# Performance work log

Measured on AMD Instinct MI355X. Metric: run time of the kernel, lower is better.

## Reference

```python
import jax, jax.numpy as jnp
import numpy as np
import math

C = 64
SCALE = 1.0 / math.sqrt(C * 9)  # BaseConv2d: 1/sqrt(in_channel*k^2), k=3


def _conv(x, w, b=None, pad=0):
    out = jax.lax.conv_general_dilated(
        x, w, window_strides=(1, 1), padding=[(pad, pad), (pad, pad)],
        dimension_numbers=("NCHW", "OIHW", "NCHW"))
    return out if b is None else out + b[None, :, None, None]


def _mod_conv(x, w, b, cond, pad):
    # cond: [B,1,C,1,1]. Original builds per-sample weights W*scale*cond and runs a
    # groups=B conv. Since cond scales the INPUT-channel axis and is spatially
    # constant, conv(x, W*diag(cond_b)) == conv(x*cond_b, W): identical math.
    return _conv(x * cond[:, 0], w * SCALE, b, pad)


def _resblock(x, w2, b2, cond2):
    # w2: [2,C,C,3,3], b2: [2,C], cond2: [2,B,1,C,1,1]
    r = jax.nn.relu(_mod_conv(x, w2[0], b2[0], cond2[0], 1))
    r = _mod_conv(r, w2[1], b2[1], cond2[1], 1)
    return r + x


def _mfe(x, w1, b1, w3, b3, w5, b5, cw1, cw2, fw, fb):
    lrelu = lambda z: jax.nn.leaky_relu(z, 0.01)
    x1 = _conv(lrelu(_conv(x, w1[0], b1[0], 0)), w1[1], b1[1], 0)
    x3 = _conv(lrelu(_conv(x, w3[0], b3[0], 1)), w3[1], b3[1], 1)
    x5 = _conv(lrelu(_conv(x, w5[0], b5[0], 2)), w5[1], b5[1], 2)
    # ChannelAttention: shared SE MLP (1x1 convs, no bias) on max- and avg-pooled stats
    se = lambda z: jnp.einsum("oi,bihw->bohw", cw2, jax.nn.relu(jnp.einsum("oi,bihw->bohw", cw1, z)))
    mx = jnp.max(x, axis=(2, 3), keepdims=True)
    av = jnp.mean(x, axis=(2, 3), keepdims=True)
    xll = jax.nn.sigmoid(se(mx) + se(av))  # [B,C,1,1]
    # FC1 = Linear(1,1) -> Linear(1,1) on the trailing size-1 dim; C1==C2==C3 (same module)
    Cg = fw[1] * (fw[0] * xll + fb[0]) + fb[1]
    return Cg * (x1 + x3 + x5)


def _pms(x, cf1, cf2, map_, res_w, res_b, mw1, mb1, mw3, mb3, mw5, mb5, caw1, caw2, fcw, fcb):
    conds = [cf1[i] for i in range(5)] + [cf2[i] for i in range(4)]
    mfe_after = {1: 0, 3: 1, 5: 2, 7: 3, 8: 4}
    o = x
    for i in range(9):
        o = _resblock(o, res_w[i], res_b[i], conds[i])
        if i in mfe_after:
            j = mfe_after[i]
            o = _mfe(o, mw1[j], mb1[j], mw3[j], mb3[j], mw5[j], mb5[j],
                     caw1[j], caw2[j], fcw[j], fcb[j])
    return o * map_ + x


def setup_inputs() -> dict:
    key = jax.random.key(0)
    ks = jax.random.split(key, 16)
    B, H, W = 4, 128, 128
    d = {}
    d["x"] = jax.random.normal(ks[0], (B, C, H, W), jnp.float32)
    # modulation scales ~1 (EqualLinear bias_init=1)
    d["condition_feature1"] = jax.random.uniform(ks[1], (5, 2, B, 1, C, 1, 1), jnp.float32, 0.5, 1.5)
    d["condition_feature2"] = jax.random.uniform(ks[2], (4, 2, B, 1, C, 1, 1), jnp.float32, 0.5, 1.5)
    d["map"] = jax.random.uniform(ks[3], (B, 1, H, W), jnp.float32)
    d["res_w"] = jax.random.normal(ks[4], (9, 2, C, C, 3, 3), jnp.float32)  # BaseConv2d stores raw randn weight
    d["res_b"] = jax.random.normal(ks[5], (9, 2, C), jnp.float32) * 0.01
    d["mw1"] = jax.random.normal(ks[6], (5, 2, C, C, 1, 1), jnp.float32) * (0.1 * math.sqrt(2.0 / C))
    d["mb1"] = jnp.zeros((5, 2, C), jnp.float32)
    d["mw3"] = jax.random.normal(ks[7], (5, 2, C, C, 3, 3), jnp.float32) * (0.1 * math.sqrt(2.0 / (C * 9)))
    d["mb3"] = jnp.zeros((5, 2, C), jnp.float32)
    d["mw5"] = jax.random.normal(ks[8], (5, 2, C, C, 5, 5), jnp.float32) * (0.1 * math.sqrt(2.0 / (C * 25)))
    d["mb5"] = jnp.zeros((5, 2, C), jnp.float32)
    d["caw1"] = jax.random.normal(ks[9], (5, C // 16, C), jnp.float32) * math.sqrt(2.0 / C)
    d["caw2"] = jax.random.normal(ks[10], (5, C, C // 16), jnp.float32) * math.sqrt(2.0 / (C // 16))
    d["fcw"] = jax.random.normal(ks[11], (5, 2), jnp.float32)
    d["fcb"] = jax.random.normal(ks[12], (5, 2), jnp.float32) * 0.1
    return d


def reference(x, condition_feature1, condition_feature2, map, res_w, res_b,
              mw1, mb1, mw3, mb3, mw5, mb5, caw1, caw2, fcw, fcb):
    return _pms(x, condition_feature1, condition_feature2, map, res_w, res_b,
                mw1, mb1, mw3, mb3, mw5, mb5, caw1, caw2, fcw, fcb)
```

## Files before the change

kernel.cpp:

```cpp
#include <hip/hip_runtime.h>
#include <math.h>

constexpr int B = 4, C = 64, H = 128, W = 128;
constexpr int HW = H * W;
constexpr size_t TOT   = (size_t)B * C * HW;
constexpr float SCALE  = 1.0f / 24.0f;

typedef _Float16 half8 __attribute__((ext_vector_type(8)));
typedef _Float16 half4v __attribute__((ext_vector_type(4)));
typedef float floatx4 __attribute__((ext_vector_type(4)));

constexpr size_t A_RES = 0;
constexpr size_t A_M1  = 2654208;
constexpr size_t A_M3  = 2695168;
constexpr size_t A_M5  = 3063808;
constexpr size_t A_TOT = 4087808;

__global__ __launch_bounds__(256) void wt_kernel(
    const float* __restrict__ rw, const float* __restrict__ mw1,
    const float* __restrict__ mw3, const float* __restrict__ mw5,
    const float* __restrict__ cf1, const float* __restrict__ cf2,
    _Float16* __restrict__ wt)
{
    size_t e = (size_t)blockIdx.x * 256 + threadIdx.x;
    const float* src; int K; float scale; int l;
    if (e < A_M1) {
        int cb = (int)(e / 36864); l = (int)(e - (size_t)cb * 36864);
        int conv = cb >> 2, b = cb & 3;
        src = rw + (size_t)conv * 36864; K = 3;
        int icw = l & 7, l15 = (l >> 3) & 15, q = (l >> 7) & 3;
        int mt = (l >> 9) & 3, h = (l >> 11) & 1, kk = l >> 12;
        int oc = mt * 16 + l15, ic = h * 32 + q * 8 + icw;
        int kh = kk / 3, kw = kk - kh * 3;
        float cond = (conv < 10) ? cf1[(size_t)(conv * 4 + b) * 64 + ic]
                                 : cf2[(size_t)((conv - 10) * 4 + b) * 64 + ic];
        wt[e] = (_Float16)(src[((oc * C + ic) * 3 + kh) * 3 + kw] * SCALE * cond);
        return;
    } else if (e < A_M3) {
        int e2 = (int)(e - A_M1); int conv = e2 / 4096; l = e2 - conv * 4096;
        src = mw1 + (size_t)conv * 4096; K = 1; scale = 1.f;
    } else if (e < A_M5) {
        int e2 = (int)(e - A_M3); int conv = e2 / 36864; l = e2 - conv * 36864;
        src = mw3 + (size_t)conv * 36864; K = 3; scale = 1.f;
    } else {
        int e2 = (int)(e - A_M5); int conv = e2 / 102400; l = e2 - conv * 102400;
        src = mw5 + (size_t)conv * 102400; K = 5; scale = 1.f;
    }
    int j   = l & 7;
    int l15 = (l >> 3) & 15;
    int q   = (l >> 7) & 3;
    int mt  = (l >> 9) & 3;
    int h   = (l >> 11) & 1;
    int kk  = l >> 12;
    int oc = mt * 16 + l15, ic = h * 32 + q * 8 + j;
    int kh = kk / K, kw = kk - kh * K;
    wt[e] = (_Float16)(src[((oc * C + ic) * K + kh) * K + kw] * scale);
}

__global__ __launch_bounds__(256) void xcvt_kernel(
    const float* __restrict__ x, _Float16* __restrict__ xh)
{
    __shared__ _Float16 s[64 * 72];
    const int b = blockIdx.y;
    const size_t p0 = (size_t)blockIdx.x * 64;
    const int t = threadIdx.x, px = t & 63, cg0 = t >> 6;
#pragma unroll
    for (int k = 0; k < 16; ++k) {
        int c = cg0 * 16 + k;
        s[px * 72 + c] = (_Float16)x[((size_t)(b * 64 + c)) * HW + p0 + px];
    }
    __syncthreads();
#pragma unroll
    for (int k = 0; k < 2; ++k) {
        int idx = k * 256 + t;
        int pxw = idx >> 3, o8 = idx & 7;
        uint4 v = *(const uint4*)&s[pxw * 72 + o8 * 8];
        *(uint4*)&xh[((size_t)b * HW + p0 + pxw) * 64 + o8 * 8] = v;
    }
}

__global__ __launch_bounds__(256) void init_kernel(unsigned* __restrict__ st)
{
    int i = blockIdx.x * 256 + threadIdx.x;
    if (i < 5 * 512) st[i] = 0u;
}

__device__ __forceinline__ unsigned fenc(float f) {
    unsigned b = __float_as_uint(f);
    return (b & 0x80000000u) ? ~b : (b | 0x80000000u);
}
__device__ __forceinline__ float fdec(unsigned u) {
    unsigned b = (u & 0x80000000u) ? (u & 0x7fffffffu) : ~u;
    return __uint_as_float(b);
}

__device__ __forceinline__ void loadAo(const _Float16* __restrict__ base,
                                       int og, int q, int l15, uint4* dst)
{
    const uint4* p = (const uint4*)base;
#pragma unroll
    for (int h = 0; h < 2; ++h)
#pragma unroll
        for (int m = 0; m < 2; ++m)
            dst[h * 2 + m] = p[(h * 4 + og * 2 + m) * 64 + q * 16 + l15];
}

template <int IWs, int NPXP>
__device__ __forceinline__ void mstep_og(const unsigned int* __restrict__ s_b,
    const uint4* a, floatx4 (&acc)[2][4], int ph, int l15, int q,
    int kh, int kw, int off)
{
#pragma unroll
    for (int h = 0; h < 2; ++h) {
        half8 af0 = __builtin_bit_cast(half8, a[h * 2 + 0]);
        half8 af1 = __builtin_bit_cast(half8, a[h * 2 + 1]);
#pragma unroll
        for (int ng = 0; ng < 4; ++ng) {
            int row = 4 * ph + ng + kh + off;
            int px = row * IWs + l15 + kw + off;
            half8 bf = __builtin_bit_cast(half8, ((const uint4*)s_b)[(h * 4 + q) * NPXP + px]);
            acc[0][ng] = __builtin_amdgcn_mfma_f32_16x16x32_f16(af0, bf, acc[0][ng], 0, 0, 0);
            acc[1][ng] = __builtin_amdgcn_mfma_f32_16x16x32_f16(af1, bf, acc[1][ng], 0, 0, 0);
        }
    }
}

template <bool STATS>
__global__ __launch_bounds__(512, 1) void fres_kernel(
    const _Float16* __restrict__ in, const _Float16* __restrict__ w0a,
    const _Float16* __restrict__ w1a,
    const float* __restrict__ bias0, const float* __restrict__ bias1,
    unsigned* __restrict__ umax, float* __restrict__ fsum,
    _Float16* __restrict__ out)
{
    constexpr int NIN = 401;
    constexpr int RNP = 329;
    __shared__ __align__(16) unsigned s_in[NIN * 32];
    __shared__ __align__(16) unsigned s_r[RNP * 32];
    __shared__ float s_stat[2][8][64];

    const int tid = threadIdx.x;
    const int bx = blockIdx.x, b = blockIdx.y;
    const int y0 = (bx >> 3) * 16, x0 = (bx & 7) * 16;
    const _Float16* w0 = w0a + (size_t)b * 36864;
    const _Float16* w1 = w1a + (size_t)b * 36864;
    const int lane = tid & 63, wv = tid >> 6;
    const int pg = wv & 3, og = wv >> 2;
    const int l15 = lane & 15, q = lane >> 4;

    uint4 a0[4], a1[4];
    loadAo(w0, og, q, l15, a0);

    for (int idx = tid; idx < 400 * 8; idx += 512) {
        int px = idx >> 3, o8 = idx & 7;
        int r = px / 20, cix = px - r * 20;
        int gy = y0 + r - 2, gx = x0 + cix - 2;
        uint4 v = {0u, 0u, 0u, 0u};
        if (gy >= 0 && gy < H && gx >= 0 && gx < W)
            v = *(const uint4*)&in[((size_t)b * HW + (size_t)gy * W + gx) * 64 + o8 * 8];
        ((uint4*)s_in)[o8 * NIN + px] = v;
    }
    __syncthreads();

    int spb[6], pval[6];
#pragma unroll
    for (int t = 0; t < 6; ++t) {
        int p = (pg * 6 + t) * 16 + l15;
        pval[t] = p;
        int pc = p < 324 ? p : 0;
        int jr = pc / 18, jc = pc - jr * 18;
        spb[t] = jr * 20 + jc;
    }

    floatx4 acc1[2][6] = {};
#pragma unroll
    for (int g = 0; g < 9; ++g) {
        uint4* cur = (g & 1) ? a1 : a0;
        uint4* nxt = (g & 1) ? a0 : a1;
        const _Float16* np = (g < 8) ? w0 + (size_t)(g + 1) * 4096 : w1;
        loadAo(np, og, q, l15, nxt);
        __builtin_amdgcn_sched_barrier(0);
        const int kh = g / 3, kw = g - kh * 3;
#pragma unroll
        for (int h = 0; h < 2; ++h) {
            half8 af0 = __builtin_bit_cast(half8, cur[h * 2 + 0]);
            half8 af1 = __builtin_bit_cast(half8, cur[h * 2 + 1]);
#pragma unroll
            for (int t = 0; t < 6; ++t) {
                half8 bf = __builtin_bit_cast(half8,
                    ((const uint4*)s_in)[(h * 4 + q) * NIN + spb[t] + kh * 20 + kw]);
                acc1[0][t] = __builtin_amdgcn_mfma_f32_16x16x32_f16(af0, bf, acc1[0][t], 0, 0, 0);
                acc1[1][t] = __builtin_amdgcn_mfma_f32_16x16x32_f16(af1, bf, acc1[1][t], 0, 0, 0);
            }
        }
    }

#pragma unroll
    for (int t = 0; t < 6; ++t) {
        int p = pval[t];
        if (p < 324) {
            int jr = p / 18, jc = p - jr * 18;
            bool valid = (unsigned)(y0 + jr - 1) < (unsigned)H &&
                         (unsigned)(x0 + jc - 1) < (unsigned)W;
#pragma unroll
            for (int m = 0; m < 2; ++m) {
                int oc0 = og * 32 + m * 16 + q * 4;
                float4 bv = *(const float4*)(bias0 + oc0);
                float v0 = 0.f, v1 = 0.f, v2 = 0.f, v3 = 0.f;
                if (valid) {
                    v0 = fmaxf(acc1[m][t][0] + bv.x, 0.f);
                    v1 = fmaxf(acc1[m][t][1] + bv.y, 0.f);
                    v2 = fmaxf(acc1[m][t][2] + bv.z, 0.f);
                    v3 = fmaxf(acc1[m][t][3] + bv.w, 0.f);
                }
                half4v hv = { (_Float16)v0, (_Float16)v1, (_Float16)v2, (_Float16)v3 };
                int o8r = og * 4 + m * 2 + (q >> 1);
                ((uint2*)s_r)[(o8r * RNP + p) * 2 + (q & 1)] = __builtin_bit_cast(uint2, hv);
            }
        }
    }
    __syncthreads();

    floatx4 acc2[2][4] = {};
#pragma unroll
    for (int g = 0; g < 9; ++g) {
        uint4* cur = (g & 1) ? a0 : a1;
        uint4* nxt = (g & 1) ? a1 : a0;
        if (g < 8) {
            loadAo(w1 + (size_t)(g + 1) * 4096, og, q, l15, nxt);
            __builtin_amdgcn_sched_barrier(0);
        }
        const int kh = g / 3, kw = g - kh * 3;
#pragma unroll
        for (int h = 0; h < 2; ++h) {
            half8 af0 = __builtin_bit_cast(half8, cur[h * 2 + 0]);
            half8 af1 = __builtin_bit_cast(half8, cur[h * 2 + 1]);
#pragma unroll
            for (int ng = 0; ng < 4; ++ng) {
                int sp = (pg * 4 + ng + kh) * 18 + l15 + kw;
                half8 bf = __builtin_bit_cast(half8, ((const uint4*)s_r)[(h * 4 + q) * RNP + sp]);
                acc2[0][ng] = __builtin_amdgcn_mfma_f32_16x16x32_f16(af0, bf, acc2[0][ng], 0, 0, 0);
                acc2[1][ng] = __builtin_amdgcn_mfma_f32_16x16x32_f16(af1, bf, acc2[1][ng], 0, 0, 0);
            }
        }
    }

    float lmax[2][4], lsum[2][4];
    if (STATS) {
#pragma unroll
        for (int m = 0; m < 2; ++m)
#pragma unroll
            for (int r = 0; r < 4; ++r) { lmax[m][r] = -INFINITY; lsum[m][r] = 0.f; }
    }
#pragma unroll
    for (int m = 0; m < 2; ++m) {
        const int oc0 = og * 32 + m * 16 + q * 4;
        const float4 bv = *(const float4*)(bias1 + oc0);
        const int o8r = og * 4 + m * 2 + (q >> 1);
#pragma unroll
        for (int ng = 0; ng < 4; ++ng) {
            const int row = pg * 4 + ng;
            const int spres = (row + 2) * 20 + l15 + 2;
            uint2 ru = ((const uint2*)s_in)[(o8r * NIN + spres) * 2 + (q & 1)];
            half4v rv = __builtin_bit_cast(half4v, ru);
            float v[4];
            v[0] = acc2[m][ng][0] + bv.x + (float)rv[0];
            v[1] = acc2[m][ng][1] + bv.y + (float)rv[1];
            v[2] = acc2[m][ng][2] + bv.z + (float)rv[2];
            v[3] = acc2[m][ng][3] + bv.w + (float)rv[3];
            const size_t off = ((size_t)b * HW + (size_t)(y0 + row) * W + x0 + l15) * 64 + oc0;
            half4v hv = { (_Float16)v[0], (_Float16)v[1], (_Float16)v[2], (_Float16)v[3] };
            *(half4v*)&out[off] = hv;
            if (STATS) {
#pragma unroll
                for (int r = 0; r < 4; ++r) {
                    lmax[m][r] = fmaxf(lmax[m][r], v[r]);
                    lsum[m][r] += v[r];
                }
            }
        }
    }
    if (STATS) {
#pragma unroll
        for (int msk = 1; msk < 16; msk <<= 1) {
#pragma unroll
            for (int m = 0; m < 2; ++m)
#pragma unroll
                for (int r = 0; r < 4; ++r) {
                    lmax[m][r] = fmaxf(lmax[m][r], __shfl_xor(lmax[m][r], msk));
                    lsum[m][r] += __shfl_xor(lsum[m][r], msk);
                }
        }
        if (l15 == 0) {
#pragma unroll
            for (int m = 0; m < 2; ++m)
#pragma unroll
                for (int r = 0; r < 4; ++r) {
                    int oc = og * 32 + m * 16 + q * 4 + r;
                    s_stat[0][wv][oc] = lmax[m][r];
                    s_stat[1][wv][oc] = lsum[m][r];
                }
        }
        __syncthreads();
        if (tid < 64) {
            int oc = tid;
            int w0i = (oc < 32) ? 0 : 4;
            float mv = s_stat[0][w0i][oc], sv = s_stat[1][w0i][oc];
#pragma unroll
            for (int k = 1; k < 4; ++k) {
                mv = fmaxf(mv, s_stat[0][w0i + k][oc]);
                sv += s_stat[1][w0i + k][oc];
            }
            atomicMax(&umax[b * 64 + oc], fenc(mv));
            atomicAdd(&fsum[b * 64 + oc], sv);
        }
    }
}

__global__ __launch_bounds__(256, 2) void mfe1_kernel(
    const _Float16* __restrict__ in,
    const _Float16* __restrict__ w5, const _Float16* __restrict__ w3,
    const _Float16* __restrict__ w1,
    const float* __restrict__ b5, const float* __restrict__ b3,
    const float* __restrict__ b1,
    _Float16* __restrict__ t5, _Float16* __restrict__ t3, _Float16* __restrict__ t1)
{
    constexpr int IWs = 20, NPX = 240, NPXP = 241;
    __shared__ __align__(16) unsigned int s_b[NPXP * 32];

    const int tid = threadIdx.x;
    const int bx = blockIdx.x, b = blockIdx.y;
    const int y0 = (bx >> 3) * 8, x0 = (bx & 7) * 16;
    const int lane = tid & 63, wv = tid >> 6;
    const int ph = wv & 1, og = wv >> 1;
    const int l15 = lane & 15, q = lane >> 4;

    uint4 a0[4], a1[4];
    loadAo(w5, og, q, l15, a0);

    for (int idx = tid; idx < NPX * 8; idx += 256) {
        int px = idx >> 3, o8 = idx & 7;
        int r = px / IWs, cix = px - r * IWs;
        int gy = y0 + r - 2, gx = x0 + cix - 2;
        uint4 v = {0u, 0u, 0u, 0u};
        if (gy >= 0 && gy < H && gx >= 0 && gx < W)
            v = *(const uint4*)&in[((size_t)b * HW + (size_t)gy * W + gx) * 64 + o8 * 8];
        ((uint4*)s_b)[o8 * NPXP + px] = v;
    }
    __syncthreads();

    floatx4 acc[2][4] = {};
    const floatx4 z4 = {0.f, 0.f, 0.f, 0.f};

    auto epi = [&](const float* bias, _Float16* outp, bool reset) {
#pragma unroll
        for (int m = 0; m < 2; ++m) {
            const int oc0 = og * 32 + m * 16 + q * 4;
            const float4 bv = *(const float4*)(bias + oc0);
#pragma unroll
            for (int ng = 0; ng < 4; ++ng) {
                const int y = y0 + 4 * ph + ng, x = x0 + l15;
                const size_t off = ((size_t)b * HW + (size_t)y * W + x) * 64 + oc0;
                float v[4] = { acc[m][ng][0] + bv.x, acc[m][ng][1] + bv.y,
                               acc[m][ng][2] + bv.z, acc[m][ng][3] + bv.w };
#pragma unroll
                for (int r = 0; r < 4; ++r) v[r] = v[r] > 0.f ? v[r] : 0.01f * v[r];
                half4v hv = { (_Float16)v[0], (_Float16)v[1], (_Float16)v[2], (_Float16)v[3] };
                *(half4v*)&outp[off] = hv;
                if (reset) acc[m][ng] = z4;
            }
        }
    };

#pragma unroll
    for (int g = 0; g < 25; ++g) {
        uint4* cur = (g & 1) ? a1 : a0;
        uint4* nxt = (g & 1) ? a0 : a1;
        const _Float16* np = (g + 1 < 25) ? w5 + (size_t)(g + 1) * 4096 : w3;
        loadAo(np, og, q, l15, nxt);
        __builtin_amdgcn_sched_barrier(0);
        mstep_og<IWs, NPXP>(s_b, cur, acc, ph, l15, q, g / 5, g % 5, 0);
    }
    epi(b5, t5, true);
#pragma unroll
    for (int g = 0; g < 9; ++g) {
        uint4* cur = (g & 1) ? a0 : a1;
        uint4* nxt = (g & 1) ? a1 : a0;
        const _Float16* np = (g + 1 < 9) ? w3 + (size_t)(g + 1) * 4096 : w1;
        loadAo(np, og, q, l15, nxt);
        __builtin_amdgcn_sched_barrier(0);
        mstep_og<IWs, NPXP>(s_b, cur, acc, ph, l15, q, g / 3, g % 3, 1);
    }
    epi(b3, t3, true);
    mstep_og<IWs, NPXP>(s_b, a0, acc, ph, l15, q, 0, 0, 2);
    epi(b1, t1, false);
}

__global__ __launch_bounds__(256, 2) void mfe2_kernel(
    const _Float16* __restrict__ t5in, const _Float16* __restrict__ t3in,
    const _Float16* __restrict__ t1in,
    const _Float16* __restrict__ w5, const _Float16* __restrict__ w3,
    const _Float16* __restrict__ w1,
    const float* __restrict__ b5, const float* __restrict__ b3,
    const float* __restrict__ b1,
    const unsigned* __restrict__ umax, const float* __restrict__ fsum,
    const float* __restrict__ caw1, const float* __restrict__ caw2,
    const float* __restrict__ fcwj, const float* __restrict__ fcbj,
    _Float16* __restrict__ o)
{
    constexpr int IWs = 20, NPX = 240, NPXP = 241;
    __shared__ __align__(16) unsigned int s_b[NPXP * 32];
    __shared__ float s_hid[8];

    const int tid = threadIdx.x;
    const int bx = blockIdx.x, b = blockIdx.y;
    const int y0 = (bx >> 3) * 8, x0 = (bx & 7) * 16;
    const int lane = tid & 63, wv = tid >> 6;
    const int ph = wv & 1, og = wv >> 1;
    const int l15 = lane & 15, q = lane >> 4;

    auto stageB = [&](const _Float16* __restrict__ src) {
        for (int idx = tid; idx < NPX * 8; idx += 256) {
            int px = idx >> 3, o8 = idx & 7;
            int r = px / IWs, cix = px - r * IWs;
            int gy = y0 + r - 2, gx = x0 + cix - 2;
            uint4 v = {0u, 0u, 0u, 0u};
            if (gy >= 0 && gy < H && gx >= 0 && gx < W)
                v = *(const uint4*)&src[((size_t)b * HW + (size_t)gy * W + gx) * 64 + o8 * 8];
            ((uint4*)s_b)[o8 * NPXP + px] = v;
        }
    };

    uint4 a0[4], a1[4];
    loadAo(w5, og, q, l15, a0);

    stageB(t5in);
    if (tid < 8) {
        int which = tid >> 2, hh = tid & 3;
        float s = 0.f;
        for (int i = 0; i < 64; ++i) {
            float val = which ? (fsum[b * 64 + i] * (1.f / HW)) : fdec(umax[b * 64 + i]);
            s += caw1[hh * 64 + i] * val;
        }
        s_hid[tid] = fmaxf(s, 0.f);
    }
    __syncthreads();

    floatx4 acc[2][4] = {};

#pragma unroll
    for (int g = 0; g < 25; ++g) {
        uint4* cur = (g & 1) ? a1 : a0;
        uint4* nxt = (g & 1) ? a0 : a1;
        const _Float16* np = (g + 1 < 25) ? w5 + (size_t)(g + 1) * 4096 : w3;
        loadAo(np, og, q, l15, nxt);
        __builtin_amdgcn_sched_barrier(0);
        mstep_og<IWs, NPXP>(s_b, cur, acc, ph, l15, q, g / 5, g % 5, 0);
    }
    __syncthreads();
    stageB(t3in);
    __syncthreads();
#pragma unroll
    for (int g = 0; g < 9; ++g) {
        uint4* cur = (g & 1) ? a0 : a1;
        uint4* nxt = (g & 1) ? a1 : a0;
        const _Float16* np = (g + 1 < 9) ? w3 + (size_t)(g + 1) * 4096 : w1;
        loadAo(np, og, q, l15, nxt);
        __builtin_amdgcn_sched_barrier(0);
        mstep_og<IWs, NPXP>(s_b, cur, acc, ph, l15, q, g / 3, g % 3, 1);
    }
    __syncthreads();
    stageB(t1in);
    __syncthreads();
    mstep_og<IWs, NPXP>(s_b, a0, acc, ph, l15, q, 0, 0, 2);

    float hs[4];
#pragma unroll
    for (int hh = 0; hh < 4; ++hh) hs[hh] = s_hid[hh] + s_hid[4 + hh];
    const float fw0 = fcwj[0], fw1 = fcwj[1], fb0 = fcbj[0], fb1 = fcbj[1];
#pragma unroll
    for (int m = 0; m < 2; ++m) {
        const int oc0 = og * 32 + m * 16 + q * 4;
        const float4 bv5 = *(const float4*)(b5 + oc0);
        const float4 bv3 = *(const float4*)(b3 + oc0);
        const float4 bv1 = *(const float4*)(b1 + oc0);
        float bs[4] = { bv5.x + bv3.x + bv1.x, bv5.y + bv3.y + bv1.y,
                        bv5.z + bv3.z + bv1.z, bv5.w + bv3.w + bv1.w };
        float cg[4];
#pragma unroll
        for (int r = 0; r < 4; ++r) {
            const float4 w2 = *(const float4*)(caw2 + (oc0 + r) * 4);
            float s = w2.x * hs[0] + w2.y * hs[1] + w2.z * hs[2] + w2.w * hs[3];
            float xll = 1.f / (1.f + expf(-s));
            cg[r] = fw1 * (fw0 * xll + fb0) + fb1;
        }
#pragma unroll
        for (int ng = 0; ng < 4; ++ng) {
            const int y = y0 + 4 * ph + ng, x = x0 + l15;
            const size_t off = ((size_t)b * HW + (size_t)y * W + x) * 64 + oc0;
            float v[4];
#pragma unroll
            for (int r = 0; r < 4; ++r) v[r] = (acc[m][ng][r] + bs[r]) * cg[r];
            half4v hv = { (_Float16)v[0], (_Float16)v[1], (_Float16)v[2], (_Float16)v[3] };
            *(half4v*)&o[off] = hv;
        }
    }
}

__global__ __launch_bounds__(256) void final_kernel(
    const _Float16* __restrict__ o, const float* __restrict__ mapp,
    const float* __restrict__ x, float* __restrict__ out)
{
    __shared__ _Float16 s[64 * 72];
    const int b = blockIdx.y;
    const size_t p0 = (size_t)blockIdx.x * 64;
    const int t = threadIdx.x;
#pragma unroll
    for (int k = 0; k < 2; ++k) {
        int idx = k * 256 + t;
        int pxw = idx >> 3, o8 = idx & 7;
        uint4 v = *(const uint4*)&o[((size_t)b * HW + p0 + pxw) * 64 + o8 * 8];
        *(uint4*)&s[pxw * 72 + o8 * 8] = v;
    }
    __syncthreads();
    const int px = t & 63, cg0 = t >> 6;
    const float mv = mapp[(size_t)b * HW + p0 + px];
#pragma unroll
    for (int k = 0; k < 16; ++k) {
        int c = cg0 * 16 + k;
        size_t off = ((size_t)(b * 64 + c)) * HW + p0 + px;
        out[off] = (float)s[px * 72 + c] * mv + x[off];
    }
}

extern "C" void kernel_launch(void* const* d_in, const int* in_sizes, int n_in,
                              void* d_out, int out_size, void* d_ws, size_t ws_size,
                              hipStream_t stream)
{
    const float* x    = (const float*)d_in[0];
    const float* cf1  = (const float*)d_in[1];
    const float* cf2  = (const float*)d_in[2];
    const float* mapp = (const float*)d_in[3];
    const float* rw   = (const float*)d_in[4];
    const float* rb   = (const float*)d_in[5];
    const float* mw1  = (const float*)d_in[6];
    const float* mb1  = (const float*)d_in[7];
    const float* mw3  = (const float*)d_in[8];
    const float* mb3  = (const float*)d_in[9];
    const float* mw5  = (const float*)d_in[10];
    const float* mb5  = (const float*)d_in[11];
    const float* caw1 = (const float*)d_in[12];
    const float* caw2 = (const float*)d_in[13];
    const float* fcw  = (const float*)d_in[14];
    const float* fcb  = (const float*)d_in[15];
    float* out = (float*)d_out;

    _Float16* wta = (_Float16*)d_ws;
    _Float16* hb  = wta + A_TOT;
    _Float16* xh  = hb;
    _Float16* bA  = hb + TOT;
    _Float16* bB  = hb + 2 * TOT;
    _Float16* t5  = hb + 3 * TOT;
    _Float16* t3  = hb + 4 * TOT;
    unsigned* stat = (unsigned*)(hb + 5 * TOT);

    wt_kernel<<<dim3((unsigned)(A_TOT / 256)), 256, 0, stream>>>(rw, mw1, mw3, mw5, cf1, cf2, wta);
    init_kernel<<<dim3(10), 256, 0, stream>>>(stat);
    xcvt_kernel<<<dim3(256, B), 256, 0, stream>>>(x, xh);

    const dim3 fgrid(64, B);
    const dim3 mgrid(128, B);

    const _Float16* cur = xh;
    int mfe_j = 0;
    for (int i = 0; i < 9; ++i) {
        _Float16* nxt = (i & 1) ? bB : bA;
        bool isMfe = (i == 1 || i == 3 || i == 5 || i == 7 || i == 8);
        const _Float16* w0a = wta + A_RES + (size_t)(i * 2 + 0) * 4 * 36864;
        const _Float16* w1a = wta + A_RES + (size_t)(i * 2 + 1) * 4 * 36864;
        unsigned* um = stat + (size_t)mfe_j * 512;
        float* fs = (float*)(stat + (size_t)mfe_j * 512 + 256);
        if (isMfe)
            fres_kernel<true><<<fgrid, 512, 0, stream>>>(
                cur, w0a, w1a, rb + (i * 2 + 0) * C, rb + (i * 2 + 1) * C, um, fs, nxt);
        else
            fres_kernel<false><<<fgrid, 512, 0, stream>>>(
                cur, w0a, w1a, rb + (i * 2 + 0) * C, rb + (i * 2 + 1) * C, nullptr, nullptr, nxt);
        cur = nxt;

        if (isMfe) {
            int j = mfe_j++;
            mfe1_kernel<<<mgrid, 256, 0, stream>>>(
                cur,
                wta + A_M5 + (size_t)(j * 2 + 0) * 102400,
                wta + A_M3 + (size_t)(j * 2 + 0) * 36864,
                wta + A_M1 + (size_t)(j * 2 + 0) * 4096,
                mb5 + (j * 2 + 0) * C, mb3 + (j * 2 + 0) * C, mb1 + (j * 2 + 0) * C,
                t5, t3, xh);
            mfe2_kernel<<<mgrid, 256, 0, stream>>>(
                t5, t3, xh,
                wta + A_M5 + (size_t)(j * 2 + 1) * 102400,
                wta + A_M3 + (size_t)(j * 2 + 1) * 36864,
                wta + A_M1 + (size_t)(j * 2 + 1) * 4096,
                mb5 + (j * 2 + 1) * C, mb3 + (j * 2 + 1) * C, mb1 + (j * 2 + 1) * C,
                um, fs, caw1 + j * 4 * C, caw2 + j * C * 4,
                fcw + j * 2, fcb + j * 2, (_Float16*)cur);
        }
    }
    final_kernel<<<dim3(256, B), 256, 0, stream>>>(cur, mapp, x, out);
}
```

Baseline: 521.2 us.

## Deepen weight prefetch to three buffers and double-buffer LDS B-fragment reads

```diff
diff --git a/kernel.cpp b/kernel.cpp
--- a/kernel.cpp
+++ b/kernel.cpp
@@ -106,9 +106,21 @@
 }
 
 template <int IWs, int NPXP>
-__device__ __forceinline__ void mstep_og(const unsigned int* __restrict__ s_b,
-    const uint4* a, floatx4 (&acc)[2][4], int ph, int l15, int q,
-    int kh, int kw, int off)
+__device__ __forceinline__ void readB8(const unsigned* __restrict__ s_b,
+    int ph, int l15, int q, int kh, int kw, int off, uint4* bf)
+{
+#pragma unroll
+    for (int h = 0; h < 2; ++h)
+#pragma unroll
+        for (int ng = 0; ng < 4; ++ng) {
+            int row = 4 * ph + ng + kh + off;
+            int px = row * IWs + l15 + kw + off;
+            bf[h * 4 + ng] = ((const uint4*)s_b)[(h * 4 + q) * NPXP + px];
+        }
+}
+
+__device__ __forceinline__ void domfma_og(const uint4* a, const uint4* bf,
+                                          floatx4 (&acc)[2][4])
 {
 #pragma unroll
     for (int h = 0; h < 2; ++h) {
@@ -116,13 +128,18 @@
         half8 af1 = __builtin_bit_cast(half8, a[h * 2 + 1]);
 #pragma unroll
         for (int ng = 0; ng < 4; ++ng) {
-            int row = 4 * ph + ng + kh + off;
-            int px = row * IWs + l15 + kw + off;
-            half8 bf = __builtin_bit_cast(half8, ((const uint4*)s_b)[(h * 4 + q) * NPXP + px]);
-            acc[0][ng] = __builtin_amdgcn_mfma_f32_16x16x32_f16(af0, bf, acc[0][ng], 0, 0, 0);
-            acc[1][ng] = __builtin_amdgcn_mfma_f32_16x16x32_f16(af1, bf, acc[1][ng], 0, 0, 0);
-        }
-    }
+            half8 b = __builtin_bit_cast(half8, bf[h * 4 + ng]);
+            acc[0][ng] = __builtin_amdgcn_mfma_f32_16x16x32_f16(af0, b, acc[0][ng], 0, 0, 0);
+            acc[1][ng] = __builtin_amdgcn_mfma_f32_16x16x32_f16(af1, b, acc[1][ng], 0, 0, 0);
+        }
+    }
+}
+
+__device__ __forceinline__ void mfeParams(int g, int& kh, int& kw, int& off)
+{
+    if (g < 25)      { kh = g / 5; kw = g % 5; off = 0; }
+    else if (g < 34) { int ls = g - 25; kh = ls / 3; kw = ls % 3; off = 1; }
+    else             { kh = 0; kw = 0; off = 2; }
 }
 
 template <bool STATS>
@@ -148,8 +165,13 @@
     const int pg = wv & 3, og = wv >> 2;
     const int l15 = lane & 15, q = lane >> 4;
 
-    uint4 a0[4], a1[4];
-    loadAo(w0, og, q, l15, a0);
+    auto aPtrF = [&](int g) -> const _Float16* {
+        return (g < 9) ? w0 + (size_t)g * 4096 : w1 + (size_t)(g - 9) * 4096;
+    };
+
+    uint4 A[3][4];
+    loadAo(aPtrF(0), og, q, l15, A[0]);
+    loadAo(aPtrF(1), og, q, l15, A[1]);
 
     for (int idx = tid; idx < 400 * 8; idx += 512) {
         int px = idx >> 3, o8 = idx & 7;
@@ -175,11 +197,9 @@
     floatx4 acc1[2][6] = {};
 #pragma unroll
     for (int g = 0; g < 9; ++g) {
-        uint4* cur = (g & 1) ? a1 : a0;
-        uint4* nxt = (g & 1) ? a0 : a1;
-        const _Float16* np = (g < 8) ? w0 + (size_t)(g + 1) * 4096 : w1;
-        loadAo(np, og, q, l15, nxt);
+        loadAo(aPtrF(g + 2), og, q, l15, A[(g + 2) % 3]);
         __builtin_amdgcn_sched_barrier(0);
+        const uint4* cur = A[g % 3];
         const int kh = g / 3, kw = g - kh * 3;
 #pragma unroll
         for (int h = 0; h < 2; ++h) {
@@ -221,28 +241,28 @@
     }
     __syncthreads();
 
-    floatx4 acc2[2][4] = {};
-#pragma unroll
-    for (int g = 0; g < 9; ++g) {
-        uint4* cur = (g & 1) ? a0 : a1;
-        uint4* nxt = (g & 1) ? a1 : a0;
-        if (g < 8) {
-            loadAo(w1 + (size_t)(g + 1) * 4096, og, q, l15, nxt);
-            __builtin_amdgcn_sched_barrier(0);
-        }
-        const int kh = g / 3, kw = g - kh * 3;
-#pragma unroll
-        for (int h = 0; h < 2; ++h) {
-            half8 af0 = __builtin_bit_cast(half8, cur[h * 2 + 0]);
-            half8 af1 = __builtin_bit_cast(half8, cur[h * 2 + 1]);
+    auto readB2 = [&](int kh, int kw, uint4* bf) {
+#pragma unroll
+        for (int h = 0; h < 2; ++h)
 #pragma unroll
             for (int ng = 0; ng < 4; ++ng) {
                 int sp = (pg * 4 + ng + kh) * 18 + l15 + kw;
-                half8 bf = __builtin_bit_cast(half8, ((const uint4*)s_r)[(h * 4 + q) * RNP + sp]);
-                acc2[0][ng] = __builtin_amdgcn_mfma_f32_16x16x32_f16(af0, bf, acc2[0][ng], 0, 0, 0);
-                acc2[1][ng] = __builtin_amdgcn_mfma_f32_16x16x32_f16(af1, bf, acc2[1][ng], 0, 0, 0);
+                bf[h * 4 + ng] = ((const uint4*)s_r)[(h * 4 + q) * RNP + sp];
             }
-        }
+    };
+
+    floatx4 acc2[2][4] = {};
+    uint4 BF[2][8];
+    readB2(0, 0, BF[1]);
+#pragma unroll
+    for (int g = 9; g < 18; ++g) {
+        if (g + 2 < 18) loadAo(aPtrF(g + 2), og, q, l15, A[(g + 2) % 3]);
+        if (g + 1 < 18) {
+            int ls = g + 1 - 9;
+            readB2(ls / 3, ls % 3, BF[(g + 1) & 1]);
+        }
+        __builtin_amdgcn_sched_barrier(0);
+        domfma_og(A[g % 3], BF[g & 1], acc2);
     }
 
     float lmax[2][4], lsum[2][4];
@@ -335,8 +355,15 @@
     const int ph = wv & 1, og = wv >> 1;
     const int l15 = lane & 15, q = lane >> 4;
 
-    uint4 a0[4], a1[4];
-    loadAo(w5, og, q, l15, a0);
+    auto aPtr = [&](int g) -> const _Float16* {
+        if (g < 25) return w5 + (size_t)g * 4096;
+        if (g < 34) return w3 + (size_t)(g - 25) * 4096;
+        return w1;
+    };
+
+    uint4 A[3][4];
+    loadAo(aPtr(0), og, q, l15, A[0]);
+    loadAo(aPtr(1), og, q, l15, A[1]);
 
     for (int idx = tid; idx < NPX * 8; idx += 256) {
         int px = idx >> 3, o8 = idx & 7;
@@ -351,6 +378,8 @@
 
     floatx4 acc[2][4] = {};
     const floatx4 z4 = {0.f, 0.f, 0.f, 0.f};
+    uint4 BF[2][8];
+    readB8<IWs, NPXP>(s_b, ph, l15, q, 0, 0, 0, BF[0]);
 
     auto epi = [&](const float* bias, _Float16* outp, bool reset) {
 #pragma unroll
@@ -373,27 +402,19 @@
     };
 
 #pragma unroll
-    for (int g = 0; g < 25; ++g) {
-        uint4* cur = (g & 1) ? a1 : a0;
-        uint4* nxt = (g & 1) ? a0 : a1;
-        const _Float16* np = (g + 1 < 25) ? w5 + (size_t)(g + 1) * 4096 : w3;
-        loadAo(np, og, q, l15, nxt);
+    for (int g = 0; g < 35; ++g) {
+        if (g + 2 < 35) loadAo(aPtr(g + 2), og, q, l15, A[(g + 2) % 3]);
+        if (g + 1 < 35) {
+            int kh, kw, off;
+            mfeParams(g + 1, kh, kw, off);
+            readB8<IWs, NPXP>(s_b, ph, l15, q, kh, kw, off, BF[(g + 1) & 1]);
+        }
         __builtin_amdgcn_sched_barrier(0);
-        mstep_og<IWs, NPXP>(s_b, cur, acc, ph, l15, q, g / 5, g % 5, 0);
-    }
-    epi(b5, t5, true);
-#pragma unroll
-    for (int g = 0; g < 9; ++g) {
-        uint4* cur = (g & 1) ? a0 : a1;
-        uint4* nxt = (g & 1) ? a1 : a0;
-        const _Float16* np = (g + 1 < 9) ? w3 + (size_t)(g + 1) * 4096 : w1;
-        loadAo(np, og, q, l15, nxt);
-        __builtin_amdgcn_sched_barrier(0);
-        mstep_og<IWs, NPXP>(s_b, cur, acc, ph, l15, q, g / 3, g % 3, 1);
-    }
-    epi(b3, t3, true);
-    mstep_og<IWs, NPXP>(s_b, a0, acc, ph, l15, q, 0, 0, 2);
-    epi(b1, t1, false);
+        domfma_og(A[g % 3], BF[g & 1], acc);
+        if (g == 24)      epi(b5, t5, true);
+        else if (g == 33) epi(b3, t3, true);
+        else if (g == 34) epi(b1, t1, false);
+    }
 }
 
 __global__ __launch_bounds__(256, 2) void mfe2_kernel(
@@ -431,8 +452,15 @@
         }
     };
 
-    uint4 a0[4], a1[4];
-    loadAo(w5, og, q, l15, a0);
+    auto aPtr = [&](int g) -> const _Float16* {
+        if (g < 25) return w5 + (size_t)g * 4096;
+        if (g < 34) return w3 + (size_t)(g - 25) * 4096;
+        return w1;
+    };
+
+    uint4 A[3][4];
+    loadAo(aPtr(0), og, q, l15, A[0]);
+    loadAo(aPtr(1), og, q, l15, A[1]);
 
     stageB(t5in);
     if (tid < 8) {
@@ -447,32 +475,36 @@
     __syncthreads();
 
     floatx4 acc[2][4] = {};
-
+    uint4 BF[2][8];
+
+    readB8<IWs, NPXP>(s_b, ph, l15, q, 0, 0, 0, BF[0]);
 #pragma unroll
     for (int g = 0; g < 25; ++g) {
-        uint4* cur = (g & 1) ? a1 : a0;
-        uint4* nxt = (g & 1) ? a0 : a1;
-        const _Float16* np = (g + 1 < 25) ? w5 + (size_t)(g + 1) * 4096 : w3;
-        loadAo(np, og, q, l15, nxt);
+        loadAo(aPtr(g + 2), og, q, l15, A[(g + 2) % 3]);
+        if (g + 1 < 25)
+            readB8<IWs, NPXP>(s_b, ph, l15, q, (g + 1) / 5, (g + 1) % 5, 0, BF[(g + 1) & 1]);
         __builtin_amdgcn_sched_barrier(0);
-        mstep_og<IWs, NPXP>(s_b, cur, acc, ph, l15, q, g / 5, g % 5, 0);
+        domfma_og(A[g % 3], BF[g & 1], acc);
     }
     __syncthreads();
     stageB(t3in);
     __syncthreads();
-#pragma unroll
-    for (int g = 0; g < 9; ++g) {
-        uint4* cur = (g & 1) ? a0 : a1;
-        uint4* nxt = (g & 1) ? a1 : a0;
-        const _Float16* np = (g + 1 < 9) ? w3 + (size_t)(g + 1) * 4096 : w1;
-        loadAo(np, og, q, l15, nxt);
+    readB8<IWs, NPXP>(s_b, ph, l15, q, 0, 0, 1, BF[1]);
+#pragma unroll
+    for (int g = 25; g < 34; ++g) {
+        if (g + 2 < 35) loadAo(aPtr(g + 2), og, q, l15, A[(g + 2) % 3]);
+        if (g + 1 < 34) {
+            int ls = g + 1 - 25;
+            readB8<IWs, NPXP>(s_b, ph, l15, q, ls / 3, ls % 3, 1, BF[(g + 1) & 1]);
+        }
         __builtin_amdgcn_sched_barrier(0);
-        mstep_og<IWs, NPXP>(s_b, cur, acc, ph, l15, q, g / 3, g % 3, 1);
+        domfma_og(A[g % 3], BF[g & 1], acc);
     }
     __syncthreads();
     stageB(t1in);
     __syncthreads();
-    mstep_og<IWs, NPXP>(s_b, a0, acc, ph, l15, q, 0, 0, 2);
+    readB8<IWs, NPXP>(s_b, ph, l15, q, 0, 0, 2, BF[0]);
+    domfma_og(A[34 % 3], BF[0], acc);
 
     float hs[4];
 #pragma unroll
```

Measured after the change: 1.641 ms. +214.8%, slower.
